# Kernel tuning notes

Hardware: AMD Instinct MI355X
Metric: run time of the kernel (lower is better)

Reference implementation:

```python
import jax, jax.numpy as jnp
import numpy as np

B, L, D = 4, 4096, 1024
K = D // 4

def setup_inputs() -> dict:
    key = jax.random.key(0)
    ks = jax.random.split(key, 16)
    def w(k, sh):
        return jax.random.normal(k, sh, dtype=jnp.float32) * 0.02
    return {
        'x': jax.random.normal(ks[0], (B, L, D), dtype=jnp.float32),
        'Wk1': w(ks[1], (D, D)), 'bk1': jnp.zeros((D,), jnp.float32),
        'Wk2': w(ks[2], (D, K * 4)), 'bk2': jnp.zeros((K * 4,), jnp.float32),
        'Wq1': w(ks[3], (D, D)), 'bq1': jnp.zeros((D,), jnp.float32),
        'Wq2': w(ks[4], (D, K * 4)), 'bq2': jnp.zeros((K * 4,), jnp.float32),
        'Wv': w(ks[5], (D, D)), 'bv': jnp.zeros((D,), jnp.float32),
        'gamma': jnp.ones((D,), jnp.float32), 'beta': jnp.zeros((D,), jnp.float32),
        'Wo': w(ks[6], (D, D)), 'bo': jnp.zeros((D,), jnp.float32),
    }

def _normalize(q, eps=1e-12):
    n = jnp.sqrt(jnp.sum(q * q, axis=-1, keepdims=True))
    return q / jnp.maximum(n, eps)

def _quat_conj(q):
    return q * jnp.asarray([1., -1., -1., -1.], dtype=q.dtype)

def _quat_mul(q1, q2):
    w1, x1, y1, z1 = q1[..., 0], q1[..., 1], q1[..., 2], q1[..., 3]
    w2, x2, y2, z2 = q2[..., 0], q2[..., 1], q2[..., 2], q2[..., 3]
    w = w1 * w2 - x1 * x2 - y1 * y2 - z1 * z2
    x = w1 * x2 + x1 * w2 + y1 * z2 - z1 * y2
    y = w1 * y2 - x1 * z2 + y1 * w2 + z1 * x2
    z = w1 * z2 + x1 * y2 - y1 * x2 + z1 * w2
    return jnp.stack([w, x, y, z], axis=-1)

def _quat_rotate(q, v):
    return _quat_mul(_quat_mul(q, v), _quat_conj(q))

def _mlp(x, W1, b1, W2, b2):
    h = jax.nn.gelu(x @ W1 + b1, approximate=False)
    return h @ W2 + b2

def _layernorm(x, g, b, eps=1e-5):
    mu = jnp.mean(x, axis=-1, keepdims=True)
    var = jnp.var(x, axis=-1, keepdims=True)
    return (x - mu) * jax.lax.rsqrt(var + eps) * g + b

def reference(x, Wk1, bk1, Wk2, bk2, Wq1, bq1, Wq2, bq2, Wv, bv, gamma, beta, Wo, bo):
    b, l, d = x.shape
    k = d // 4
    key_q = _normalize(_mlp(x, Wk1, bk1, Wk2, bk2).reshape(b, l, k, 4))
    query_q = _normalize(_mlp(x, Wq1, bq1, Wq2, bq2).reshape(b, l, k, 4))
    value = (x @ Wv + bv).reshape(b, l, k, 4)
    rotated = _quat_rotate(key_q, value)            # [B,L,K,4]
    memory = jnp.cumsum(rotated, axis=1)            # prefix-sum memory
    retrieved = _quat_rotate(_quat_conj(query_q), memory).reshape(b, l, d)
    norm = jnp.sqrt(jnp.arange(1, l + 1, dtype=x.dtype)).reshape(1, l, 1)
    out = _layernorm(retrieved / norm, gamma, beta) @ Wo + bo
    return x + out
```

## Files before the change

### kernel.cpp

```cpp
#include <hip/hip_runtime.h>
#include <cstddef>
#include <cstdint>

static constexpr int Bb  = 4;
static constexpr int Ll  = 4096;
static constexpr int Mm  = 16384;
static constexpr int KK  = 1024;
static constexpr int NCH = 128;
static constexpr int CHL = 32;

typedef __attribute__((ext_vector_type(8))) short short8;
typedef __attribute__((ext_vector_type(4))) float f32x4;

#define AS1C(p) ((const __attribute__((address_space(1))) void*)(p))
#define AS3(p)  ((__attribute__((address_space(3))) void*)(p))

__device__ __forceinline__ float b2f(unsigned short u) {
    union { unsigned int i; float f; } c; c.i = ((unsigned int)u) << 16; return c.f;
}
__device__ __forceinline__ unsigned short f2b(float f) {
    union { float f; unsigned int i; } c; c.f = f;
    unsigned int r = c.i + 0x7fffu + ((c.i >> 16) & 1u);
    return (unsigned short)(r >> 16);
}
__device__ __forceinline__ float4 bq2f(ushort4 u) {
    return make_float4(b2f(u.x), b2f(u.y), b2f(u.z), b2f(u.w));
}
__device__ __forceinline__ ushort4 f2bq(float4 v) {
    ushort4 o; o.x = f2b(v.x); o.y = f2b(v.y); o.z = f2b(v.z); o.w = f2b(v.w); return o;
}
__device__ __forceinline__ float4 qmul(const float4 a, const float4 b) {
    float4 r;
    r.x = a.x * b.x - a.y * b.y - a.z * b.z - a.w * b.w;
    r.y = a.x * b.y + a.y * b.x + a.z * b.w - a.w * b.z;
    r.z = a.x * b.z - a.y * b.w + a.z * b.x + a.w * b.y;
    r.w = a.x * b.w + a.y * b.z - a.z * b.y + a.w * b.x;
    return r;
}
__device__ __forceinline__ float4 qconj(const float4 a) {
    return make_float4(a.x, -a.y, -a.z, -a.w);
}
__device__ __forceinline__ float4 qnorm(const float4 a) {
    float n = sqrtf(a.x * a.x + a.y * a.y + a.z * a.z + a.w * a.w);
    float inv = 1.0f / fmaxf(n, 1e-12f);
    return make_float4(a.x * inv, a.y * inv, a.z * inv, a.w * inv);
}
__device__ __forceinline__ float gelu_fast(float v) {
    const float a = fabsf(v) * 0.70710678118654752f;
    const float t = 1.0f / (1.0f + 0.3275911f * a);
    const float p = t * (0.254829592f + t * (-0.284496736f + t * (1.421413741f
                   + t * (-1.453152027f + t * 1.061405429f))));
    const float e = __expf(-a * a);
    const float erfa = 1.0f - p * e;
    return 0.5f * v * (1.0f + copysignf(erfa, v));
}

__global__ __launch_bounds__(256)
void conv_k(const float* __restrict__ src, unsigned short* __restrict__ dst, int n4)
{
    const int i = blockIdx.x * 256 + threadIdx.x;
    if (i >= n4) return;
    const float4 v = reinterpret_cast<const float4*>(src)[i];
    reinterpret_cast<ushort4*>(dst)[i] = f2bq(v);
}

__global__ __launch_bounds__(256)
void wtrans_k(const float* __restrict__ src, unsigned short* __restrict__ dst)
{
    __shared__ float t[32][33];
    const int tx = threadIdx.x, ty = threadIdx.y;
    const int n0 = blockIdx.x * 32, k0 = blockIdx.y * 32;
    #pragma unroll
    for (int j = ty; j < 32; j += 8)
        t[j][tx] = src[(size_t)(k0 + j) * 1024 + n0 + tx];
    __syncthreads();
    #pragma unroll
    for (int j = ty; j < 32; j += 8)
        dst[(size_t)(n0 + j) * 1024 + k0 + tx] = f2b(t[tx][j]);
}

__global__ __launch_bounds__(256)
void bcat_k(const float* __restrict__ bk1, const float* __restrict__ bq1,
            const float* __restrict__ bv,  const float* __restrict__ bk2,
            const float* __restrict__ bq2, float* __restrict__ b1,
            float* __restrict__ b2)
{
    const int i = blockIdx.x * 256 + threadIdx.x;
    if (i < 3072) b1[i] = (i < 1024) ? bk1[i] : (i < 2048 ? bq1[i - 1024] : bv[i - 2048]);
    if (i < 2048) b2[i] = (i < 1024) ? bk2[i] : bq2[i - 1024];
}

template<int MODE>
__global__ __launch_bounds__(512, 2)
void gemm256_k(const unsigned short* __restrict__ A, int astride,
               const unsigned short* __restrict__ BT,
               const float* __restrict__ bias,
               const float* __restrict__ resid,
               unsigned short* __restrict__ outH,
               unsigned short* __restrict__ outV,
               float* __restrict__ outF,
               int Nn)
{
    extern __shared__ char smem[];
    const int tid  = threadIdx.x;
    const int lane = tid & 63;
    const int w    = tid >> 6;
    const int wr   = w >> 2;
    const int wc   = w & 3;

    const int nwg = gridDim.x;
    const int cpx = nwg >> 3;
    const int bid = blockIdx.x;
    const int swz = (bid & 7) * cpx + (bid >> 3);
    const int nTN = Nn >> 8;
    const int m0  = (swz / nTN) << 8;
    const int n0  = (swz % nTN) << 8;
    const int aoff = (MODE == 1 && n0 >= 1024) ? 1024 : 0;

    const unsigned short* pA[2];
    const unsigned short* pB[2];
    #pragma unroll
    for (int c2 = 0; c2 < 2; ++c2) {
        const int s = c2 * 512 + tid;
        const int line = s >> 3;
        const int v = (s & 7) ^ (line & 7);
        const int r = 2 * line + (v >> 2);
        const int kcs = v & 3;
        pA[c2] = A + (size_t)(m0 + r) * astride + aoff + kcs * 8;
        pB[c2] = BT + (size_t)(n0 + r) * KK + kcs * 8;
    }

    auto STAGE = [&](int matB, int slot, int kh, int koff) {
        #pragma unroll
        for (int c2 = 0; c2 < 2; ++c2) {
            __builtin_amdgcn_global_load_lds(
                AS1C((matB ? pB[c2] : pA[c2]) + koff),
                AS3(smem + matB * 65536 + slot * 32768 + kh * 16384 + c2 * 8192 + w * 1024),
                16, 0, 0);
        }
    };

    const int kc = lane >> 4;
    const int rl = lane & 15;
    int offA[8], offB[4];
    #pragma unroll
    for (int mi = 0; mi < 8; ++mi) {
        const int r = wr * 128 + mi * 16 + rl;
        offA[mi] = (r >> 1) * 128 + (((((r & 1) << 2) | kc) ^ ((r >> 1) & 7)) << 4);
    }
    #pragma unroll
    for (int ni = 0; ni < 4; ++ni) {
        const int r = wc * 64 + ni * 16 + rl;
        offB[ni] = (r >> 1) * 128 + (((((r & 1) << 2) | kc) ^ ((r >> 1) & 7)) << 4);
    }

    f32x4 acc[8][4] = {};
    short8 af[8];

    auto PHASE = [&](int slot, int kh, int nih, int smat, int sslot, int skh,
                     int skoff, int vm) {
        const int ub = slot * 32768 + kh * 16384;
        if (nih == 0) {
            #pragma unroll
            for (int mi = 0; mi < 8; ++mi)
                af[mi] = *(const short8*)(smem + ub + offA[mi]);
        }
        const short8 b0 = *(const short8*)(smem + 65536 + ub + offB[2 * nih + 0]);
        const short8 b1 = *(const short8*)(smem + 65536 + ub + offB[2 * nih + 1]);
        if (smat >= 0) STAGE(smat, sslot, skh, skoff);
        __builtin_amdgcn_s_barrier();
        __builtin_amdgcn_s_setprio(1);
        #pragma unroll
        for (int mi = 0; mi < 8; ++mi) {
            acc[mi][2 * nih + 0] = __builtin_amdgcn_mfma_f32_16x16x32_bf16(af[mi], b0, acc[mi][2 * nih + 0], 0, 0, 0);
            acc[mi][2 * nih + 1] = __builtin_amdgcn_mfma_f32_16x16x32_bf16(af[mi], b1, acc[mi][2 * nih + 1], 0, 0, 0);
        }
        __builtin_amdgcn_s_setprio(0);
        if (vm == 4)      asm volatile("s_waitcnt vmcnt(4)" ::: "memory");
        else if (vm == 0) asm volatile("s_waitcnt vmcnt(0)" ::: "memory");
        __builtin_amdgcn_s_barrier();
    };

    STAGE(0, 0, 0, 0);  STAGE(1, 0, 0, 0);
    STAGE(0, 0, 1, 32); STAGE(1, 0, 1, 32);
    STAGE(0, 1, 0, 64); STAGE(1, 1, 0, 64);
    asm volatile("s_waitcnt vmcnt(4)" ::: "memory");
    __builtin_amdgcn_s_barrier();

    for (int i = 0; i < 7; ++i) {
        const int kb = i * 128;
        PHASE(0, 0, 0,  0, 1, 1, kb + 96,  -1);
        PHASE(0, 0, 1,  1, 1, 1, kb + 96,  -1);
        PHASE(0, 1, 0,  0, 0, 0, kb + 128, -1);
        PHASE(0, 1, 1,  1, 0, 0, kb + 128,  4);
        PHASE(1, 0, 0,  0, 0, 1, kb + 160, -1);
        PHASE(1, 0, 1,  1, 0, 1, kb + 160, -1);
        PHASE(1, 1, 0,  0, 1, 0, kb + 192, -1);
        PHASE(1, 1, 1,  1, 1, 0, kb + 192,  4);
    }
    PHASE(0, 0, 0,  0, 1, 1, 992, -1);
    PHASE(0, 0, 1,  1, 1, 1, 992, -1);
    PHASE(0, 1, 0, -1, 0, 0, 0,   -1);
    PHASE(0, 1, 1, -1, 0, 0, 0,    0);
    PHASE(1, 0, 0, -1, 0, 0, 0,   -1);
    PHASE(1, 0, 1, -1, 0, 0, 0,   -1);
    PHASE(1, 1, 0, -1, 0, 0, 0,   -1);
    PHASE(1, 1, 1, -1, 0, 0, 0,   -1);
    __syncthreads();

    const int colb = n0 + wc * 64 + rl;
    float bv[4];
    #pragma unroll
    for (int ni = 0; ni < 4; ++ni) bv[ni] = bias[colb + ni * 16];

    if (MODE == 2) {
        const int rowb = m0 + wr * 128 + kc * 4;
        #pragma unroll
        for (int ni = 0; ni < 4; ++ni) {
            const int col = colb + ni * 16;
            #pragma unroll
            for (int mi = 0; mi < 8; ++mi) {
                #pragma unroll
                for (int rr = 0; rr < 4; ++rr) {
                    const int row = rowb + mi * 16 + rr;
                    const size_t ix = (size_t)row * 1024 + col;
                    outF[ix] = acc[mi][ni][rr] + bv[ni] + resid[ix];
                }
            }
        }
    } else {
        const bool dogelu = (MODE == 0) && (n0 < 2048);
        unsigned short* dst;
        int stride, col0;
        if (MODE == 0 && n0 >= 2048) { dst = outV; stride = 1024; col0 = n0 - 2048; }
        else                         { dst = outH; stride = 2048; col0 = n0; }
        unsigned short* eb = (unsigned short*)smem;
        const int er = tid >> 2, eq = tid & 3;
        #pragma unroll
        for (int pass = 0; pass < 2; ++pass) {
            if (wr == pass) {
                #pragma unroll
                for (int ni = 0; ni < 4; ++ni) {
                    const int col = wc * 64 + ni * 16 + rl;
                    #pragma unroll
                    for (int mi = 0; mi < 8; ++mi) {
                        #pragma unroll
                        for (int rr = 0; rr < 4; ++rr) {
                            float v = acc[mi][ni][rr] + bv[ni];
                            if (dogelu) v = gelu_fast(v);
                            eb[(mi * 16 + kc * 4 + rr) * 264 + col] = f2b(v);
                        }
                    }
                }
            }
            __syncthreads();
            const size_t grow = (size_t)(m0 + pass * 128 + er) * stride + col0 + eq * 64;
            #pragma unroll
            for (int j = 0; j < 8; ++j)
                *(uint4*)(dst + grow + j * 8) = *(const uint4*)(eb + er * 264 + eq * 64 + j * 8);
            __syncthreads();
        }
    }
}

__global__ __launch_bounds__(256)
void rotfuse_k(const unsigned short* __restrict__ qb2, unsigned short* __restrict__ valb,
               float* __restrict__ part)
{
    const int idx = blockIdx.x * 256 + threadIdx.x;
    const int kq  = idx & 255;
    const int ch  = (idx >> 8) & 127;
    const int b   = idx >> 15;
    const int row0 = b * Ll + ch * CHL;
    float4 s = make_float4(0.f, 0.f, 0.f, 0.f);
    for (int i = 0; i < CHL; ++i) {
        const int row = row0 + i;
        const float4 q = qnorm(bq2f(*reinterpret_cast<const ushort4*>(qb2 + (size_t)row * 2048 + kq * 4)));
        ushort4* vp = reinterpret_cast<ushort4*>(valb + (size_t)row * 1024 + kq * 4);
        const float4 r = qmul(qmul(q, bq2f(*vp)), qconj(q));
        *vp = f2bq(r);
        s.x += r.x; s.y += r.y; s.z += r.z; s.w += r.w;
    }
    *reinterpret_cast<float4*>(part + (size_t)idx * 4) = s;
}

__global__ __launch_bounds__(256)
void scan2_k(float* __restrict__ part)
{
    const int idx = blockIdx.x * 256 + threadIdx.x;
    const int kq = idx & 255, b = idx >> 8;
    float4 run = make_float4(0.f, 0.f, 0.f, 0.f);
    for (int c = 0; c < NCH; ++c) {
        float4* p = reinterpret_cast<float4*>(part + (((size_t)(b * NCH + c)) * 256 + kq) * 4);
        const float4 t = *p;
        *p = run;
        run.x += t.x; run.y += t.y; run.z += t.z; run.w += t.w;
    }
}

__global__ __launch_bounds__(256)
void scan3ln_k(const unsigned short* __restrict__ rotb, const float* __restrict__ part,
               const unsigned short* __restrict__ qb2,
               const float* __restrict__ gamma, const float* __restrict__ beta,
               unsigned short* __restrict__ ln)
{
    const int kq = threadIdx.x;
    const int ch = blockIdx.x & (NCH - 1);
    const int b  = blockIdx.x >> 7;
    const int row0 = b * Ll + ch * CHL;
    float4 run = *reinterpret_cast<const float4*>(part + (((size_t)(b * NCH + ch)) * 256 + kq) * 4);

    __shared__ float red[2][2][4];
    const int wid = kq >> 6, lane = kq & 63;
    const float4 g4 = *reinterpret_cast<const float4*>(gamma + kq * 4);
    const float4 b4 = *reinterpret_cast<const float4*>(beta  + kq * 4);

    for (int i = 0; i < CHL; ++i) {
        const int row = row0 + i;
        const float4 v = bq2f(*reinterpret_cast<const ushort4*>(rotb + (size_t)row * 1024 + kq * 4));
        run.x += v.x; run.y += v.y; run.z += v.z; run.w += v.w;

        const float4 q = qnorm(bq2f(*reinterpret_cast<const ushort4*>(qb2 + (size_t)row * 2048 + 1024 + kq * 4)));
        float4 r = qmul(qmul(qconj(q), run), q);
        const float inv = rsqrtf((float)(ch * CHL + i + 1));
        r.x *= inv; r.y *= inv; r.z *= inv; r.w *= inv;

        float s  = r.x + r.y + r.z + r.w;
        float ss = r.x * r.x + r.y * r.y + r.z * r.z + r.w * r.w;
        #pragma unroll
        for (int off = 32; off > 0; off >>= 1) {
            s  += __shfl_xor(s, off);
            ss += __shfl_xor(ss, off);
        }
        if (lane == 0) { red[i & 1][0][wid] = s; red[i & 1][1][wid] = ss; }
        __syncthreads();
        const float sum = red[i & 1][0][0] + red[i & 1][0][1] + red[i & 1][0][2] + red[i & 1][0][3];
        const float ssq = red[i & 1][1][0] + red[i & 1][1][1] + red[i & 1][1][2] + red[i & 1][1][3];
        const float mu  = sum * (1.0f / 1024.0f);
        const float var = ssq * (1.0f / 1024.0f) - mu * mu;
        const float sc  = rsqrtf(var + 1e-5f);

        float4 o;
        o.x = (r.x - mu) * sc * g4.x + b4.x;
        o.y = (r.y - mu) * sc * g4.y + b4.y;
        o.z = (r.z - mu) * sc * g4.z + b4.z;
        o.w = (r.w - mu) * sc * g4.w + b4.w;
        *reinterpret_cast<ushort4*>(ln + (size_t)row * 1024 + kq * 4) = f2bq(o);
    }
}

extern "C" void kernel_launch(void* const* d_in, const int* in_sizes, int n_in,
                              void* d_out, int out_size, void* d_ws, size_t ws_size,
                              hipStream_t stream)
{
    const float* x     = (const float*)d_in[0];
    const float* Wk1   = (const float*)d_in[1];
    const float* bk1   = (const float*)d_in[2];
    const float* Wk2   = (const float*)d_in[3];
    const float* bk2   = (const float*)d_in[4];
    const float* Wq1   = (const float*)d_in[5];
    const float* bq1   = (const float*)d_in[6];
    const float* Wq2   = (const float*)d_in[7];
    const float* bq2   = (const float*)d_in[8];
    const float* Wv    = (const float*)d_in[9];
    const float* bv    = (const float*)d_in[10];
    const float* gamma = (const float*)d_in[11];
    const float* beta  = (const float*)d_in[12];
    const float* Wo    = (const float*)d_in[13];
    const float* bo    = (const float*)d_in[14];
    float* out = (float*)d_out;

    const size_t TD = (size_t)Mm * 1024;
    const size_t DD = (size_t)1024 * 1024;

    unsigned short* qb2   = (unsigned short*)d_ws;
    unsigned short* xb    = qb2;
    unsigned short* wcat1 = qb2 + TD;
    unsigned short* h     = qb2 + 2 * TD;
    unsigned short* valb  = h + 2 * TD;
    unsigned short* wcat2 = valb + TD;
    unsigned short* woT   = wcat2 + 2 * DD;
    float*          bcat1 = (float*)(woT + DD);
    float*          bcat2 = bcat1 + 3072;
    float*          part  = bcat2 + 2048;

    const dim3 blk(256);
    const dim3 tblk(32, 8);
    const dim3 tgrid(32, 32);

    (void)hipFuncSetAttribute((const void*)gemm256_k<0>, hipFuncAttributeMaxDynamicSharedMemorySize, 131072);
    (void)hipFuncSetAttribute((const void*)gemm256_k<1>, hipFuncAttributeMaxDynamicSharedMemorySize, 131072);
    (void)hipFuncSetAttribute((const void*)gemm256_k<2>, hipFuncAttributeMaxDynamicSharedMemorySize, 131072);

    conv_k<<<(int)(TD / 4 / 256), blk, 0, stream>>>(x, xb, (int)(TD / 4));
    wtrans_k<<<tgrid, tblk, 0, stream>>>(Wk1, wcat1);
    wtrans_k<<<tgrid, tblk, 0, stream>>>(Wq1, wcat1 + DD);
    wtrans_k<<<tgrid, tblk, 0, stream>>>(Wv,  wcat1 + 2 * DD);
    wtrans_k<<<tgrid, tblk, 0, stream>>>(Wk2, wcat2);
    wtrans_k<<<tgrid, tblk, 0, stream>>>(Wq2, wcat2 + DD);
    wtrans_k<<<tgrid, tblk, 0, stream>>>(Wo,  woT);
    bcat_k<<<12, blk, 0, stream>>>(bk1, bq1, bv, bk2, bq2, bcat1, bcat2);

    gemm256_k<0><<<64 * 12, 512, 131072, stream>>>(xb, 1024, wcat1, bcat1, nullptr, h, valb, nullptr, 3072);
    gemm256_k<1><<<64 * 8, 512, 131072, stream>>>(h, 2048, wcat2, bcat2, nullptr, qb2, nullptr, nullptr, 2048);

    rotfuse_k<<<(Bb * NCH * 256) / 256, blk, 0, stream>>>(qb2, valb, part);
    scan2_k<<<4, blk, 0, stream>>>(part);
    scan3ln_k<<<Bb * NCH, blk, 0, stream>>>(valb, part, qb2, gamma, beta, h);

    gemm256_k<2><<<64 * 4, 512, 131072, stream>>>(h, 1024, woT, bo, x, nullptr, nullptr, out, 1024);
}
```

Measured before the change: 457.3 us.

## Replace 256x256 GEMM tiles with 128x128 double-buffered tiles and static LDS

Swaps the 512-thread 256x256 GEMM with an 8-phase hand-scheduled pipeline for a 256-thread 128x128 GEMM. The new kernel uses a simple two-buffer K loop of 32-wide steps and 32KB of static shared memory, with launch bounds allowing three blocks per CU. The aim is more resident blocks, more blocks per launch and better load balance across CUs. In exchange it loses per-tile operand reuse, so global and LDS traffic per FLOP roughly doubles, and it waits on vmcnt(0) every step, which limits load/compute overlap.

After: 463.8 us. No clear change (+1.4%).

```diff
diff --git a/kernel.cpp b/kernel.cpp
--- a/kernel.cpp
+++ b/kernel.cpp
@@ -91,8 +91,8 @@
 }
 
 template<int MODE>
-__global__ __launch_bounds__(512, 2)
-void gemm256_k(const unsigned short* __restrict__ A, int astride,
+__global__ __launch_bounds__(256, 3)
+void gemm128_k(const unsigned short* __restrict__ A, int astride,
                const unsigned short* __restrict__ BT,
                const float* __restrict__ bias,
                const float* __restrict__ resid,
@@ -101,112 +101,86 @@
                float* __restrict__ outF,
                int Nn)
 {
-    extern __shared__ char smem[];
+    __shared__ char smem[32768];
     const int tid  = threadIdx.x;
     const int lane = tid & 63;
     const int w    = tid >> 6;
-    const int wr   = w >> 2;
-    const int wc   = w & 3;
+    const int wr   = w >> 1;
+    const int wc   = w & 1;
 
     const int nwg = gridDim.x;
     const int cpx = nwg >> 3;
     const int bid = blockIdx.x;
     const int swz = (bid & 7) * cpx + (bid >> 3);
-    const int nTN = Nn >> 8;
-    const int m0  = (swz / nTN) << 8;
-    const int n0  = (swz % nTN) << 8;
+    const int nTN = Nn >> 7;
+    const int m0  = (swz / nTN) << 7;
+    const int n0  = (swz % nTN) << 7;
     const int aoff = (MODE == 1 && n0 >= 1024) ? 1024 : 0;
 
-    const unsigned short* pA[2];
-    const unsigned short* pB[2];
+    const unsigned short* gA[2];
+    const unsigned short* gB[2];
     #pragma unroll
     for (int c2 = 0; c2 < 2; ++c2) {
-        const int s = c2 * 512 + tid;
+        const int s = c2 * 256 + tid;
         const int line = s >> 3;
-        const int v = (s & 7) ^ (line & 7);
-        const int r = 2 * line + (v >> 2);
-        const int kcs = v & 3;
-        pA[c2] = A + (size_t)(m0 + r) * astride + aoff + kcs * 8;
-        pB[c2] = BT + (size_t)(n0 + r) * KK + kcs * 8;
-    }
-
-    auto STAGE = [&](int matB, int slot, int kh, int koff) {
-        #pragma unroll
-        for (int c2 = 0; c2 < 2; ++c2) {
-            __builtin_amdgcn_global_load_lds(
-                AS1C((matB ? pB[c2] : pA[c2]) + koff),
-                AS3(smem + matB * 65536 + slot * 32768 + kh * 16384 + c2 * 8192 + w * 1024),
-                16, 0, 0);
-        }
+        const int u = (s & 7) ^ (line & 7);
+        const int r = 2 * line + (u >> 2);
+        const int kcs = u & 3;
+        gA[c2] = A + (size_t)(m0 + r) * astride + aoff + kcs * 8;
+        gB[c2] = BT + (size_t)(n0 + r) * KK + kcs * 8;
+    }
+
+    auto STAGE = [&](int c, int koff) {
+        #pragma unroll
+        for (int c2 = 0; c2 < 2; ++c2)
+            __builtin_amdgcn_global_load_lds(AS1C(gA[c2] + koff),
+                AS3(smem + c * 16384 + c2 * 4096 + w * 1024), 16, 0, 0);
+        #pragma unroll
+        for (int c2 = 0; c2 < 2; ++c2)
+            __builtin_amdgcn_global_load_lds(AS1C(gB[c2] + koff),
+                AS3(smem + c * 16384 + 8192 + c2 * 4096 + w * 1024), 16, 0, 0);
     };
 
-    const int kc = lane >> 4;
-    const int rl = lane & 15;
-    int offA[8], offB[4];
-    #pragma unroll
-    for (int mi = 0; mi < 8; ++mi) {
-        const int r = wr * 128 + mi * 16 + rl;
-        offA[mi] = (r >> 1) * 128 + (((((r & 1) << 2) | kc) ^ ((r >> 1) & 7)) << 4);
+    const int kc4 = lane >> 4;
+    const int rl  = lane & 15;
+    int offA[4], offB[4];
+    #pragma unroll
+    for (int mi = 0; mi < 4; ++mi) {
+        const int r = wr * 64 + mi * 16 + rl;
+        offA[mi] = (r >> 1) * 128 + (((((r & 1) << 2) | kc4) ^ ((r >> 1) & 7)) << 4);
     }
     #pragma unroll
     for (int ni = 0; ni < 4; ++ni) {
         const int r = wc * 64 + ni * 16 + rl;
-        offB[ni] = (r >> 1) * 128 + (((((r & 1) << 2) | kc) ^ ((r >> 1) & 7)) << 4);
-    }
-
-    f32x4 acc[8][4] = {};
-    short8 af[8];
-
-    auto PHASE = [&](int slot, int kh, int nih, int smat, int sslot, int skh,
-                     int skoff, int vm) {
-        const int ub = slot * 32768 + kh * 16384;
-        if (nih == 0) {
-            #pragma unroll
-            for (int mi = 0; mi < 8; ++mi)
-                af[mi] = *(const short8*)(smem + ub + offA[mi]);
-        }
-        const short8 b0 = *(const short8*)(smem + 65536 + ub + offB[2 * nih + 0]);
-        const short8 b1 = *(const short8*)(smem + 65536 + ub + offB[2 * nih + 1]);
-        if (smat >= 0) STAGE(smat, sslot, skh, skoff);
+        offB[ni] = 8192 + (r >> 1) * 128 + (((((r & 1) << 2) | kc4) ^ ((r >> 1) & 7)) << 4);
+    }
+
+    f32x4 acc[4][4] = {};
+
+    STAGE(0, 0);
+    asm volatile("s_waitcnt vmcnt(0)" ::: "memory");
+    __builtin_amdgcn_s_barrier();
+
+    #pragma unroll 1
+    for (int t = 0; t < 32; ++t) {
+        const int cb = (t & 1) * 16384;
+        short8 af[4], bf[4];
+        #pragma unroll
+        for (int mi = 0; mi < 4; ++mi) af[mi] = *(const short8*)(smem + cb + offA[mi]);
+        #pragma unroll
+        for (int ni = 0; ni < 4; ++ni) bf[ni] = *(const short8*)(smem + cb + offB[ni]);
+        if (t < 31) STAGE((t + 1) & 1, (t + 1) * 32);
         __builtin_amdgcn_s_barrier();
         __builtin_amdgcn_s_setprio(1);
         #pragma unroll
-        for (int mi = 0; mi < 8; ++mi) {
-            acc[mi][2 * nih + 0] = __builtin_amdgcn_mfma_f32_16x16x32_bf16(af[mi], b0, acc[mi][2 * nih + 0], 0, 0, 0);
-            acc[mi][2 * nih + 1] = __builtin_amdgcn_mfma_f32_16x16x32_bf16(af[mi], b1, acc[mi][2 * nih + 1], 0, 0, 0);
-        }
+        for (int mi = 0; mi < 4; ++mi)
+            #pragma unroll
+            for (int ni = 0; ni < 4; ++ni)
+                acc[mi][ni] = __builtin_amdgcn_mfma_f32_16x16x32_bf16(af[mi], bf[ni], acc[mi][ni], 0, 0, 0);
         __builtin_amdgcn_s_setprio(0);
-        if (vm == 4)      asm volatile("s_waitcnt vmcnt(4)" ::: "memory");
-        else if (vm == 0) asm volatile("s_waitcnt vmcnt(0)" ::: "memory");
+        if (t < 31) asm volatile("s_waitcnt vmcnt(0)" ::: "memory");
         __builtin_amdgcn_s_barrier();
-    };
-
-    STAGE(0, 0, 0, 0);  STAGE(1, 0, 0, 0);
-    STAGE(0, 0, 1, 32); STAGE(1, 0, 1, 32);
-    STAGE(0, 1, 0, 64); STAGE(1, 1, 0, 64);
-    asm volatile("s_waitcnt vmcnt(4)" ::: "memory");
-    __builtin_amdgcn_s_barrier();
-
-    for (int i = 0; i < 7; ++i) {
-        const int kb = i * 128;
-        PHASE(0, 0, 0,  0, 1, 1, kb + 96,  -1);
-        PHASE(0, 0, 1,  1, 1, 1, kb + 96,  -1);
-        PHASE(0, 1, 0,  0, 0, 0, kb + 128, -1);
-        PHASE(0, 1, 1,  1, 0, 0, kb + 128,  4);
-        PHASE(1, 0, 0,  0, 0, 1, kb + 160, -1);
-        PHASE(1, 0, 1,  1, 0, 1, kb + 160, -1);
-        PHASE(1, 1, 0,  0, 1, 0, kb + 192, -1);
-        PHASE(1, 1, 1,  1, 1, 0, kb + 192,  4);
-    }
-    PHASE(0, 0, 0,  0, 1, 1, 992, -1);
-    PHASE(0, 0, 1,  1, 1, 1, 992, -1);
-    PHASE(0, 1, 0, -1, 0, 0, 0,   -1);
-    PHASE(0, 1, 1, -1, 0, 0, 0,    0);
-    PHASE(1, 0, 0, -1, 0, 0, 0,   -1);
-    PHASE(1, 0, 1, -1, 0, 0, 0,   -1);
-    PHASE(1, 1, 0, -1, 0, 0, 0,   -1);
-    PHASE(1, 1, 1, -1, 0, 0, 0,   -1);
-    __syncthreads();
+    }
 
     const int colb = n0 + wc * 64 + rl;
     float bv[4];
@@ -214,12 +188,12 @@
     for (int ni = 0; ni < 4; ++ni) bv[ni] = bias[colb + ni * 16];
 
     if (MODE == 2) {
-        const int rowb = m0 + wr * 128 + kc * 4;
+        const int rowb = m0 + wr * 64 + kc4 * 4;
         #pragma unroll
         for (int ni = 0; ni < 4; ++ni) {
             const int col = colb + ni * 16;
             #pragma unroll
-            for (int mi = 0; mi < 8; ++mi) {
+            for (int mi = 0; mi < 4; ++mi) {
                 #pragma unroll
                 for (int rr = 0; rr < 4; ++rr) {
                     const int row = rowb + mi * 16 + rr;
@@ -235,7 +209,6 @@
         if (MODE == 0 && n0 >= 2048) { dst = outV; stride = 1024; col0 = n0 - 2048; }
         else                         { dst = outH; stride = 2048; col0 = n0; }
         unsigned short* eb = (unsigned short*)smem;
-        const int er = tid >> 2, eq = tid & 3;
         #pragma unroll
         for (int pass = 0; pass < 2; ++pass) {
             if (wr == pass) {
@@ -243,21 +216,23 @@
                 for (int ni = 0; ni < 4; ++ni) {
                     const int col = wc * 64 + ni * 16 + rl;
                     #pragma unroll
-                    for (int mi = 0; mi < 8; ++mi) {
+                    for (int mi = 0; mi < 4; ++mi) {
                         #pragma unroll
                         for (int rr = 0; rr < 4; ++rr) {
                             float v = acc[mi][ni][rr] + bv[ni];
                             if (dogelu) v = gelu_fast(v);
-                            eb[(mi * 16 + kc * 4 + rr) * 264 + col] = f2b(v);
+                            eb[(mi * 16 + kc4 * 4 + rr) * 136 + col] = f2b(v);
                         }
                     }
                 }
             }
             __syncthreads();
-            const size_t grow = (size_t)(m0 + pass * 128 + er) * stride + col0 + eq * 64;
+            const int row = tid >> 2;
+            const int cc  = (tid & 3) * 32;
+            const size_t grow = (size_t)(m0 + pass * 64 + row) * stride + col0 + cc;
             #pragma unroll
-            for (int j = 0; j < 8; ++j)
-                *(uint4*)(dst + grow + j * 8) = *(const uint4*)(eb + er * 264 + eq * 64 + j * 8);
+            for (int j = 0; j < 4; ++j)
+                *(uint4*)(dst + grow + j * 8) = *(const uint4*)(eb + row * 136 + cc + j * 8);
             __syncthreads();
         }
     }
@@ -388,10 +363,6 @@
     const dim3 tblk(32, 8);
     const dim3 tgrid(32, 32);
 
-    (void)hipFuncSetAttribute((const void*)gemm256_k<0>, hipFuncAttributeMaxDynamicSharedMemorySize, 131072);
-    (void)hipFuncSetAttribute((const void*)gemm256_k<1>, hipFuncAttributeMaxDynamicSharedMemorySize, 131072);
-    (void)hipFuncSetAttribute((const void*)gemm256_k<2>, hipFuncAttributeMaxDynamicSharedMemorySize, 131072);
-
     conv_k<<<(int)(TD / 4 / 256), blk, 0, stream>>>(x, xb, (int)(TD / 4));
     wtrans_k<<<tgrid, tblk, 0, stream>>>(Wk1, wcat1);
     wtrans_k<<<tgrid, tblk, 0, stream>>>(Wq1, wcat1 + DD);
@@ -401,12 +372,12 @@
     wtrans_k<<<tgrid, tblk, 0, stream>>>(Wo,  woT);
     bcat_k<<<12, blk, 0, stream>>>(bk1, bq1, bv, bk2, bq2, bcat1, bcat2);
 
-    gemm256_k<0><<<64 * 12, 512, 131072, stream>>>(xb, 1024, wcat1, bcat1, nullptr, h, valb, nullptr, 3072);
-    gemm256_k<1><<<64 * 8, 512, 131072, stream>>>(h, 2048, wcat2, bcat2, nullptr, qb2, nullptr, nullptr, 2048);
+    gemm128_k<0><<<128 * 24, blk, 0, stream>>>(xb, 1024, wcat1, bcat1, nullptr, h, valb, nullptr, 3072);
+    gemm128_k<1><<<128 * 16, blk, 0, stream>>>(h, 2048, wcat2, bcat2, nullptr, qb2, nullptr, nullptr, 2048);
 
     rotfuse_k<<<(Bb * NCH * 256) / 256, blk, 0, stream>>>(qb2, valb, part);
     scan2_k<<<4, blk, 0, stream>>>(part);
     scan3ln_k<<<Bb * NCH, blk, 0, stream>>>(valb, part, qb2, gamma, beta, h);
 
-    gemm256_k<2><<<64 * 4, 512, 131072, stream>>>(h, 1024, woT, bo, x, nullptr, nullptr, out, 1024);
-}
+    gemm128_k<2><<<128 * 8, blk, 0, stream>>>(h, 1024, woT, bo, x, nullptr, nullptr, out, 1024);
+}
```

## Restructure GEMM phases to split by M-half with deeper prefetch

Applied to the files above, without the earlier changes.

Reorganizes the 256x256 bf16 MFMA GEMM inner loop so each phase loads all four B fragments once and half of the A fragments, issuing 16 MFMAs per phase instead of 16 with different operand reuse. The staging schedule is reshuffled so one more async global->LDS stage is in flight (vmcnt 6 instead of 4), and an explicit lgkmcnt wait plus sched_barrier separates LDS reads from MFMAs. Launch bounds drop the min-blocks hint from 2 to 1, freeing registers but risking lower occupancy, and the main loop is no longer unrolled.

Result: no change. 459.7 us (+0.5%).

```diff
diff --git a/kernel.cpp b/kernel.cpp
--- a/kernel.cpp
+++ b/kernel.cpp
@@ -91,7 +91,7 @@
 }
 
 template<int MODE>
-__global__ __launch_bounds__(512, 2)
+__global__ __launch_bounds__(512, 1)
 void gemm256_k(const unsigned short* __restrict__ A, int astride,
                const unsigned short* __restrict__ BT,
                const float* __restrict__ bias,
@@ -123,89 +123,100 @@
     for (int c2 = 0; c2 < 2; ++c2) {
         const int s = c2 * 512 + tid;
         const int line = s >> 3;
-        const int v = (s & 7) ^ (line & 7);
-        const int r = 2 * line + (v >> 2);
-        const int kcs = v & 3;
+        const int u = (s & 7) ^ (line & 7);
+        const int r = 2 * line + (u >> 2);
+        const int kcs = u & 3;
         pA[c2] = A + (size_t)(m0 + r) * astride + aoff + kcs * 8;
         pB[c2] = BT + (size_t)(n0 + r) * KK + kcs * 8;
     }
 
-    auto STAGE = [&](int matB, int slot, int kh, int koff) {
+    auto STAGE = [&](int matB, int sbuf, int skh, int koff) {
         #pragma unroll
         for (int c2 = 0; c2 < 2; ++c2) {
             __builtin_amdgcn_global_load_lds(
                 AS1C((matB ? pB[c2] : pA[c2]) + koff),
-                AS3(smem + matB * 65536 + slot * 32768 + kh * 16384 + c2 * 8192 + w * 1024),
+                AS3(smem + matB * 65536 + sbuf * 32768 + skh * 16384 + c2 * 8192 + w * 1024),
                 16, 0, 0);
         }
     };
 
-    const int kc = lane >> 4;
-    const int rl = lane & 15;
+    const int kc4 = lane >> 4;
+    const int rl  = lane & 15;
     int offA[8], offB[4];
     #pragma unroll
-    for (int mi = 0; mi < 8; ++mi) {
-        const int r = wr * 128 + mi * 16 + rl;
-        offA[mi] = (r >> 1) * 128 + (((((r & 1) << 2) | kc) ^ ((r >> 1) & 7)) << 4);
-    }
+    for (int mh = 0; mh < 2; ++mh)
+        #pragma unroll
+        for (int mi = 0; mi < 4; ++mi) {
+            const int r = wr * 128 + mh * 64 + mi * 16 + rl;
+            offA[mh * 4 + mi] = (r >> 1) * 128 + (((((r & 1) << 2) | kc4) ^ ((r >> 1) & 7)) << 4);
+        }
     #pragma unroll
     for (int ni = 0; ni < 4; ++ni) {
         const int r = wc * 64 + ni * 16 + rl;
-        offB[ni] = (r >> 1) * 128 + (((((r & 1) << 2) | kc) ^ ((r >> 1) & 7)) << 4);
+        offB[ni] = (r >> 1) * 128 + (((((r & 1) << 2) | kc4) ^ ((r >> 1) & 7)) << 4);
     }
 
     f32x4 acc[8][4] = {};
-    short8 af[8];
-
-    auto PHASE = [&](int slot, int kh, int nih, int smat, int sslot, int skh,
+    short8 af[4], bf[4];
+
+    auto PHASE = [&](int buf, int kh, int mh, int smat, int sbuf, int skh,
                      int skoff, int vm) {
-        const int ub = slot * 32768 + kh * 16384;
-        if (nih == 0) {
+        const int ub = buf * 32768 + kh * 16384;
+        if (mh == 0) {
             #pragma unroll
-            for (int mi = 0; mi < 8; ++mi)
-                af[mi] = *(const short8*)(smem + ub + offA[mi]);
-        }
-        const short8 b0 = *(const short8*)(smem + 65536 + ub + offB[2 * nih + 0]);
-        const short8 b1 = *(const short8*)(smem + 65536 + ub + offB[2 * nih + 1]);
-        if (smat >= 0) STAGE(smat, sslot, skh, skoff);
+            for (int ni = 0; ni < 4; ++ni)
+                bf[ni] = *(const short8*)(smem + 65536 + ub + offB[ni]);
+        }
+        #pragma unroll
+        for (int mi = 0; mi < 4; ++mi)
+            af[mi] = *(const short8*)(smem + ub + offA[mh * 4 + mi]);
+        if (smat >= 0) STAGE(smat, sbuf, skh, skoff);
         __builtin_amdgcn_s_barrier();
+        asm volatile("s_waitcnt lgkmcnt(0)" ::: "memory");
+        __builtin_amdgcn_sched_barrier(0);
         __builtin_amdgcn_s_setprio(1);
         #pragma unroll
-        for (int mi = 0; mi < 8; ++mi) {
-            acc[mi][2 * nih + 0] = __builtin_amdgcn_mfma_f32_16x16x32_bf16(af[mi], b0, acc[mi][2 * nih + 0], 0, 0, 0);
-            acc[mi][2 * nih + 1] = __builtin_amdgcn_mfma_f32_16x16x32_bf16(af[mi], b1, acc[mi][2 * nih + 1], 0, 0, 0);
-        }
+        for (int mi = 0; mi < 4; ++mi)
+            #pragma unroll
+            for (int ni = 0; ni < 4; ++ni)
+                acc[mh * 4 + mi][ni] = __builtin_amdgcn_mfma_f32_16x16x32_bf16(
+                    af[mi], bf[ni], acc[mh * 4 + mi][ni], 0, 0, 0);
         __builtin_amdgcn_s_setprio(0);
-        if (vm == 4)      asm volatile("s_waitcnt vmcnt(4)" ::: "memory");
+        if (vm == 6)      asm volatile("s_waitcnt vmcnt(6)" ::: "memory");
         else if (vm == 0) asm volatile("s_waitcnt vmcnt(0)" ::: "memory");
         __builtin_amdgcn_s_barrier();
     };
 
-    STAGE(0, 0, 0, 0);  STAGE(1, 0, 0, 0);
-    STAGE(0, 0, 1, 32); STAGE(1, 0, 1, 32);
-    STAGE(0, 1, 0, 64); STAGE(1, 1, 0, 64);
-    asm volatile("s_waitcnt vmcnt(4)" ::: "memory");
+    STAGE(0, 0, 0, 0);
+    STAGE(1, 0, 0, 0);
+    STAGE(0, 0, 1, 32);
+    STAGE(1, 0, 1, 32);
+    STAGE(0, 1, 0, 64);
+    STAGE(1, 1, 0, 64);
+    STAGE(1, 1, 1, 96);
+    asm volatile("s_waitcnt vmcnt(6)" ::: "memory");
     __builtin_amdgcn_s_barrier();
 
+    #pragma unroll 1
     for (int i = 0; i < 7; ++i) {
-        const int kb = i * 128;
-        PHASE(0, 0, 0,  0, 1, 1, kb + 96,  -1);
-        PHASE(0, 0, 1,  1, 1, 1, kb + 96,  -1);
-        PHASE(0, 1, 0,  0, 0, 0, kb + 128, -1);
-        PHASE(0, 1, 1,  1, 0, 0, kb + 128,  4);
-        PHASE(1, 0, 0,  0, 0, 1, kb + 160, -1);
-        PHASE(1, 0, 1,  1, 0, 1, kb + 160, -1);
-        PHASE(1, 1, 0,  0, 1, 0, kb + 192, -1);
-        PHASE(1, 1, 1,  1, 1, 0, kb + 192,  4);
-    }
-    PHASE(0, 0, 0,  0, 1, 1, 992, -1);
-    PHASE(0, 0, 1,  1, 1, 1, 992, -1);
-    PHASE(0, 1, 0, -1, 0, 0, 0,   -1);
-    PHASE(0, 1, 1, -1, 0, 0, 0,    0);
-    PHASE(1, 0, 0, -1, 0, 0, 0,   -1);
-    PHASE(1, 0, 1, -1, 0, 0, 0,   -1);
-    PHASE(1, 1, 0, -1, 0, 0, 0,   -1);
-    PHASE(1, 1, 1, -1, 0, 0, 0,   -1);
+        const int k1 = (2 * i + 1) * 64, k2 = (2 * i + 2) * 64, k3 = (2 * i + 3) * 64;
+        PHASE(0, 0, 0,  0, 1, 1, k1 + 32, -1);
+        PHASE(0, 0, 1,  1, 0, 0, k2,      -1);
+        PHASE(0, 1, 0,  0, 0, 0, k2,      -1);
+        PHASE(0, 1, 1,  1, 0, 1, k2 + 32,  6);
+        PHASE(1, 0, 0,  0, 0, 1, k2 + 32, -1);
+        PHASE(1, 0, 1,  1, 1, 0, k3,      -1);
+        PHASE(1, 1, 0,  0, 1, 0, k3,      -1);
+        PHASE(1, 1, 1,  1, 1, 1, k3 + 32,  6);
+    }
+    PHASE(0, 0, 0,  0, 1, 1, 15 * 64 + 32, -1);
+    PHASE(0, 0, 1, -1, 0, 0, 0, -1);
+    PHASE(0, 1, 0, -1, 0, 0, 0, -1);
+    PHASE(0, 1, 1, -1, 0, 0, 0,  0);
+    PHASE(1, 0, 0, -1, 0, 0, 0, -1);
+    PHASE(1, 0, 1, -1, 0, 0, 0, -1);
+    PHASE(1, 1, 0, -1, 0, 0, 0, -1);
+    PHASE(1, 1, 1, -1, 0, 0, 0, -1);
     __syncthreads();
 
     const int colb = n0 + wc * 64 + rl;
@@ -214,17 +225,17 @@
     for (int ni = 0; ni < 4; ++ni) bv[ni] = bias[colb + ni * 16];
 
     if (MODE == 2) {
-        const int rowb = m0 + wr * 128 + kc * 4;
+        const int rowb = m0 + wr * 128 + kc4 * 4;
         #pragma unroll
         for (int ni = 0; ni < 4; ++ni) {
             const int col = colb + ni * 16;
             #pragma unroll
-            for (int mi = 0; mi < 8; ++mi) {
+            for (int fi = 0; fi < 8; ++fi) {
                 #pragma unroll
                 for (int rr = 0; rr < 4; ++rr) {
-                    const int row = rowb + mi * 16 + rr;
+                    const int row = rowb + fi * 16 + rr;
                     const size_t ix = (size_t)row * 1024 + col;
-                    outF[ix] = acc[mi][ni][rr] + bv[ni] + resid[ix];
+                    outF[ix] = acc[fi][ni][rr] + bv[ni] + resid[ix];
                 }
             }
         }
@@ -243,12 +254,12 @@
                 for (int ni = 0; ni < 4; ++ni) {
                     const int col = wc * 64 + ni * 16 + rl;
                     #pragma unroll
-                    for (int mi = 0; mi < 8; ++mi) {
+                    for (int fi = 0; fi < 8; ++fi) {
                         #pragma unroll
                         for (int rr = 0; rr < 4; ++rr) {
-                            float v = acc[mi][ni][rr] + bv[ni];
+                            float v = acc[fi][ni][rr] + bv[ni];
                             if (dogelu) v = gelu_fast(v);
-                            eb[(mi * 16 + kc * 4 + rr) * 264 + col] = f2b(v);
+                            eb[(fi * 16 + kc4 * 4 + rr) * 264 + col] = f2b(v);
                         }
                     }
                 }
```
